# Kernel optimization log

Hardware: AMD Instinct MI355X
Metric: run time of the kernel (lower is better)

The kernel has to match this reference:

```python
import jax, jax.numpy as jnp
import numpy as np

B, T, D, H = 2, 2048, 1024, 16
DH = D // H


def setup_inputs() -> dict:
    key = jax.random.key(0)
    ks = jax.random.split(key, 8)
    s = 1.0 / np.sqrt(D)  # xavier-ish scale
    return {
        "query": jax.random.normal(ks[0], (B, T, D), jnp.float32),
        "key": jax.random.normal(ks[1], (B, T, D), jnp.float32),
        "value": jax.random.normal(ks[2], (B, T, D), jnp.float32),
        "Wq": jax.random.normal(ks[3], (D, D), jnp.float32) * s,
        "bq": jnp.zeros((D,), jnp.float32),
        "Wk": jax.random.normal(ks[4], (D, D), jnp.float32) * s,
        "bk": jnp.zeros((D,), jnp.float32),
        "Wv": jax.random.normal(ks[5], (D, D), jnp.float32) * s,
        "bv": jnp.zeros((D,), jnp.float32),
        "Wo": jax.random.normal(ks[6], (D, D), jnp.float32) * s,
        "bo": jnp.zeros((D,), jnp.float32),
        # causal mask (B, T, T); True = attend
        "mask": jnp.broadcast_to(jnp.tril(jnp.ones((T, T), bool)), (B, T, T)),
    }


def _split_heads(x):  # (B, T, D) -> (B, H, T, Dh)
    return x.reshape(B, T, H, DH).transpose(0, 2, 1, 3)


def reference(query, key, value, Wq, bq, Wk, bk, Wv, bv, Wo, bo, mask):
    q = _split_heads(query @ Wq + bq)
    k = _split_heads(key @ Wk + bk)
    v = _split_heads(value @ Wv + bv)
    scores = jnp.einsum("bhqd,bhkd->bhqk", q, k) / jnp.sqrt(jnp.float32(DH))
    scores = jnp.where(mask[:, None, :, :], scores, -jnp.inf)
    w = jax.nn.softmax(scores, axis=-1)
    out = jnp.einsum("bhqk,bhkd->bhqd", w, v)
    out = out.transpose(0, 2, 1, 3).reshape(B, T, D)  # merge heads
    return out @ Wo + bo
```

## Files before the change

kernel.cpp:

```cpp
#include <hip/hip_runtime.h>

typedef unsigned short u16;
typedef __attribute__((ext_vector_type(4))) float f32x4;
typedef __attribute__((ext_vector_type(8))) short bf16x8;

#define MFMA16(a,b,c) __builtin_amdgcn_mfma_f32_16x16x32_bf16((a),(b),(c),0,0,0)

__device__ inline u16 f2bf(float f){
  union { float f; unsigned u; } v; v.f = f;
  unsigned r = v.u + 0x7FFFu + ((v.u >> 16) & 1u);
  return (u16)(r >> 16);
}
__device__ inline void storeC(float* p, float v){ *p = v; }
__device__ inline void storeC(u16* p, float v){ *p = f2bf(v); }

typedef const __attribute__((address_space(1))) unsigned int* gas_ptr;
typedef __attribute__((address_space(3))) unsigned int* las_ptr;
__device__ inline void gload_lds16(const u16* g, u16* l){
  __builtin_amdgcn_global_load_lds((gas_ptr)(const void*)g, (las_ptr)(void*)l, 16, 0, 0);
}

template<int N>
__device__ inline float rorf(float v){
  union { float f; int i; } a, b; a.f = v;
  b.i = __builtin_amdgcn_update_dpp(a.i, a.i, 0x120|N, 0xF, 0xF, false);
  return b.f;
}
__device__ inline float redMax16(float v){
  v = fmaxf(v, rorf<8>(v)); v = fmaxf(v, rorf<4>(v));
  v = fmaxf(v, rorf<2>(v)); v = fmaxf(v, rorf<1>(v));
  return v;
}
__device__ inline float redSum16(float v){
  v += rorf<8>(v); v += rorf<4>(v); v += rorf<2>(v); v += rorf<1>(v);
  return v;
}

struct CvtArgs { const float* x[3]; u16* y[3]; };
__global__ void k_cvt3(CvtArgs a, int n4){
  const float* x = a.x[blockIdx.y];
  u16* y = a.y[blockIdx.y];
  int i = blockIdx.x*blockDim.x + threadIdx.x;
  if (i < n4){
    float4 v = ((const float4*)x)[i];
    ushort4 o;
    o.x = f2bf(v.x); o.y = f2bf(v.y); o.z = f2bf(v.z); o.w = f2bf(v.w);
    ((ushort4*)y)[i] = o;
  }
}

struct TwbArgs { const float* W[4]; u16* Wt[4]; };
__global__ void k_twb4(TwbArgs a){
  __shared__ u16 t[32][33];
  const float* W = a.W[blockIdx.z];
  u16* Wt = a.Wt[blockIdx.z];
  int kb = blockIdx.x*32, nb = blockIdx.y*32;
  int tx = threadIdx.x, ty = threadIdx.y;
  #pragma unroll
  for (int i=0;i<32;i+=8)
    t[ty+i][tx] = f2bf(W[(size_t)(kb+ty+i)*1024 + nb+tx]);
  __syncthreads();
  #pragma unroll
  for (int i=0;i<32;i+=8)
    Wt[(size_t)(nb+ty+i)*1024 + kb+tx] = t[tx][ty+i];
}

__global__ void k_tv(const u16* __restrict__ V, u16* __restrict__ VT){
  __shared__ u16 t[32][33];
  int tb = blockIdx.x*32;
  int db = blockIdx.y*32;
  int bh = blockIdx.z;
  int b = bh>>4, h = bh&15;
  int tx = threadIdx.x, ty = threadIdx.y;
  #pragma unroll
  for (int i=0;i<32;i+=8)
    t[ty+i][tx] = V[(size_t)(b*2048 + tb+ty+i)*1024 + h*64 + db+tx];
  __syncthreads();
  #pragma unroll
  for (int i=0;i<32;i+=8)
    VT[(size_t)(bh*64 + db+ty+i)*2048 + tb+tx] = t[tx][ty+i];
}

template<typename OutT>
__device__ inline void gemm_body(const u16* __restrict__ A, const u16* __restrict__ Bt,
                                 const float* __restrict__ bias, OutT* __restrict__ C,
                                 int bx, int by){
  const int N=1024, K=1024;
  __shared__ __attribute__((aligned(16))) u16 As[128*64];
  __shared__ __attribute__((aligned(16))) u16 Bs[128*64];
  const int tid  = threadIdx.x;
  const int wave = tid>>6, lane = tid&63;
  const int lo = lane&15, hi = lane>>4;
  const int row0 = bx*128, col0 = by*128;
  const int wm = (wave>>1)*64, wn = (wave&1)*64;
  f32x4 acc[4][4];
  #pragma unroll
  for (int i=0;i<4;i++)
    #pragma unroll
    for (int j=0;j<4;j++) acc[i][j] = (f32x4){0.f,0.f,0.f,0.f};

  for (int k0=0; k0<K; k0+=64){
    #pragma unroll
    for (int r=0;r<4;r++){
      int c = r*256 + tid;
      gload_lds16(A  + (size_t)(row0 + (c>>3))*K + k0 + (c&7)*8, As + c*8);
      gload_lds16(Bt + (size_t)(col0 + (c>>3))*K + k0 + (c&7)*8, Bs + c*8);
    }
    __syncthreads();
    __builtin_amdgcn_s_setprio(1);
    #pragma unroll
    for (int ks=0;ks<2;ks++){
      bf16x8 af[4], bfr[4];
      #pragma unroll
      for (int mf=0;mf<4;mf++)
        af[mf] = *(const bf16x8*)(As + (wm+mf*16+lo)*64 + ks*32 + hi*8);
      #pragma unroll
      for (int nf=0;nf<4;nf++)
        bfr[nf] = *(const bf16x8*)(Bs + (wn+nf*16+lo)*64 + ks*32 + hi*8);
      #pragma unroll
      for (int mf=0;mf<4;mf++)
        #pragma unroll
        for (int nf=0;nf<4;nf++)
          acc[mf][nf] = MFMA16(af[mf], bfr[nf], acc[mf][nf]);
    }
    __builtin_amdgcn_s_setprio(0);
    __syncthreads();
  }
  #pragma unroll
  for (int mf=0;mf<4;mf++){
    #pragma unroll
    for (int nf=0;nf<4;nf++){
      int r0 = row0 + wm + mf*16 + hi*4;
      int c0 = col0 + wn + nf*16 + lo;
      float bb = bias[c0];
      #pragma unroll
      for (int r=0;r<4;r++)
        storeC(&C[(size_t)(r0+r)*N + c0], acc[mf][nf][r] + bb);
    }
  }
}

struct GemmArgs3 { const u16* A[3]; const u16* Bt[3]; const float* bias[3]; u16* C[3]; };
__global__ __launch_bounds__(256) void k_gemm3(GemmArgs3 g){
  int flat = blockIdx.x + (blockIdx.y<<5) + (blockIdx.z<<8);
  int swz = (flat&7)*96 + (flat>>3);
  int by = swz & 7, bx = (swz>>3) & 31, bz = swz >> 8;
  gemm_body<u16>(g.A[bz], g.Bt[bz], g.bias[bz], g.C[bz], bx, by);
}
__global__ __launch_bounds__(256) void k_gemmO(const u16* __restrict__ A, const u16* __restrict__ Bt,
                                               const float* __restrict__ bias, float* __restrict__ C){
  int flat = blockIdx.x + (blockIdx.y<<5);
  int swz = (flat&7)*32 + (flat>>3);
  int by = swz & 7, bx = swz >> 3;
  gemm_body<float>(A, Bt, bias, C, bx, by);
}

__global__ __launch_bounds__(256) void k_attn(
    const u16* __restrict__ Q, const u16* __restrict__ Kp,
    const u16* __restrict__ VT, u16* __restrict__ O)
{
  const int T=2048, D=1024, NT=32;
  __shared__ __attribute__((aligned(16))) u16 Ks[2][64*64];
  __shared__ __attribute__((aligned(16))) u16 Vs[2][64*64];
  __shared__ __attribute__((aligned(16))) u16 Plds[4][16*64];
  int flat = blockIdx.x + (blockIdx.y<<4);
  int swz = (flat&7)*64 + (flat>>3);
  const int xb = swz & 15;
  const int bh = swz >> 4;
  const int b = bh>>4, h = bh&15;
  const int tid = threadIdx.x;
  const int wave = tid>>6, lane = tid&63;
  const int lo = lane&15, hi = lane>>4;
  const float NEG = -__builtin_inff();
  const float sc = 0.125f * 1.44269504f;

  const int cof0 = ((hi    ) ^ (lo&7))*8;
  const int cof1 = ((hi + 4) ^ (lo&7))*8;

  const int c0 = tid, c1 = 256 + tid;
  const int sr0 = c0>>3, sj0 = (c0&7)^(sr0&7);
  const int sr1 = c1>>3, sj1 = (c1&7)^(sr1&7);
  const u16* Kbase = Kp + (size_t)(b*T)*D + h*64;
  const u16* Vbase = VT + (size_t)(bh*64)*T;
  const size_t kOff0 = (size_t)sr0*D + sj0*8, kOff1 = (size_t)sr1*D + sj1*8;
  const size_t vOff0 = (size_t)sr0*T + sj0*8, vOff1 = (size_t)sr1*T + sj1*8;

  for (int half=0; half<2; half++){
    const int qb = half ? (NT-1-xb) : xb;
    const int qrow0 = qb*64 + wave*16;
    const u16* Qb = Q + (size_t)(b*T + qrow0 + lo)*D + h*64;
    bf16x8 qf0 = *(const bf16x8*)(Qb + hi*8);
    bf16x8 qf1 = *(const bf16x8*)(Qb + 32 + hi*8);

    f32x4 o[4];
    #pragma unroll
    for (int nf=0;nf<4;nf++) o[nf] = (f32x4){0.f,0.f,0.f,0.f};
    float m[4], l[4];
    #pragma unroll
    for (int r=0;r<4;r++){ m[r] = NEG; l[r] = 0.f; }

    gload_lds16(Kbase + kOff0, &Ks[0][c0*8]);
    gload_lds16(Kbase + kOff1, &Ks[0][c1*8]);
    gload_lds16(Vbase + vOff0, &Vs[0][c0*8]);
    gload_lds16(Vbase + vOff1, &Vs[0][c1*8]);
    __syncthreads();

    int cur = 0;
    for (int kb=0; kb<=qb; kb++){
      if (kb < qb){
        const u16* Kt = Kbase + (size_t)(kb+1)*64*D;
        const u16* Vt = Vbase + (kb+1)*64;
        gload_lds16(Kt + kOff0, &Ks[cur^1][c0*8]);
        gload_lds16(Kt + kOff1, &Ks[cur^1][c1*8]);
        gload_lds16(Vt + vOff0, &Vs[cur^1][c0*8]);
        gload_lds16(Vt + vOff1, &Vs[cur^1][c1*8]);
      }
      const u16* Kl = Ks[cur];
      const u16* Vl = Vs[cur];
      f32x4 s[4];
      __builtin_amdgcn_s_setprio(1);
      #pragma unroll
      for (int nf=0;nf<4;nf++){
        int row = nf*16 + lo;
        bf16x8 kf0 = *(const bf16x8*)(Kl + row*64 + cof0);
        bf16x8 kf1 = *(const bf16x8*)(Kl + row*64 + cof1);
        f32x4 z = (f32x4){0.f,0.f,0.f,0.f};
        z = MFMA16(qf0, kf0, z);
        s[nf] = MFMA16(qf1, kf1, z);
      }
      __builtin_amdgcn_s_setprio(0);
      float ls[4][4];
      float pm[4] = {NEG,NEG,NEG,NEG};
      if (kb == qb){
        #pragma unroll
        for (int nf=0;nf<4;nf++){
          int col = kb*64 + nf*16 + lo;
          #pragma unroll
          for (int r=0;r<4;r++){
            int row = qrow0 + hi*4 + r;
            float v = s[nf][r]*sc;
            if (col > row) v = NEG;
            ls[nf][r] = v;
            pm[r] = fmaxf(pm[r], v);
          }
        }
      } else {
        #pragma unroll
        for (int nf=0;nf<4;nf++)
          #pragma unroll
          for (int r=0;r<4;r++){
            float v = s[nf][r]*sc;
            ls[nf][r] = v;
            pm[r] = fmaxf(pm[r], v);
          }
      }
      #pragma unroll
      for (int r=0;r<4;r++) pm[r] = redMax16(pm[r]);
      bool small = true;
      #pragma unroll
      for (int r=0;r<4;r++) small = small && (pm[r] <= m[r] + 8.f);
      const bool resc = !__all(small);
      float alpha[4];
      if (resc){
        #pragma unroll
        for (int r=0;r<4;r++){
          float mn = fmaxf(m[r], pm[r]);
          alpha[r] = __builtin_amdgcn_exp2f(m[r] - mn);
          m[r] = mn;
        }
      }
      float rs[4] = {0.f,0.f,0.f,0.f};
      #pragma unroll
      for (int nf=0;nf<4;nf++)
        #pragma unroll
        for (int r=0;r<4;r++){
          float p = __builtin_amdgcn_exp2f(ls[nf][r] - m[r]);
          rs[r] += p;
          int prow = hi*4+r, pcol = nf*16+lo;
          Plds[wave][prow*64 + (pcol ^ ((prow&7)<<3))] = f2bf(p);
        }
      #pragma unroll
      for (int r=0;r<4;r++) rs[r] = redSum16(rs[r]);
      if (resc){
        #pragma unroll
        for (int r=0;r<4;r++) l[r] = l[r]*alpha[r] + rs[r];
        #pragma unroll
        for (int nf=0;nf<4;nf++)
          #pragma unroll
          for (int r=0;r<4;r++) o[nf][r] *= alpha[r];
      } else {
        #pragma unroll
        for (int r=0;r<4;r++) l[r] += rs[r];
      }
      bf16x8 pa0 = *(const bf16x8*)(&Plds[wave][lo*64 + cof0]);
      bf16x8 pa1 = *(const bf16x8*)(&Plds[wave][lo*64 + cof1]);
      __builtin_amdgcn_s_setprio(1);
      #pragma unroll
      for (int nf=0;nf<4;nf++){
        int row = nf*16 + lo;
        bf16x8 v0 = *(const bf16x8*)(Vl + row*64 + cof0);
        bf16x8 v1 = *(const bf16x8*)(Vl + row*64 + cof1);
        o[nf] = MFMA16(pa0, v0, o[nf]);
        o[nf] = MFMA16(pa1, v1, o[nf]);
      }
      __builtin_amdgcn_s_setprio(0);
      __syncthreads();
      cur ^= 1;
    }
    #pragma unroll
    for (int nf=0;nf<4;nf++)
      #pragma unroll
      for (int r=0;r<4;r++){
        int row = qrow0 + hi*4 + r;
        O[(size_t)(b*T+row)*D + h*64 + nf*16 + lo] = f2bf(o[nf][r] / l[r]);
      }
  }
}

extern "C" void kernel_launch(void* const* d_in, const int* in_sizes, int n_in,
                              void* d_out, int out_size, void* d_ws, size_t ws_size,
                              hipStream_t stream) {
  const int B=2, T=2048, D=1024;
  const int M = B*T;
  const float* query = (const float*)d_in[0];
  const float* key   = (const float*)d_in[1];
  const float* value = (const float*)d_in[2];
  const float* Wq = (const float*)d_in[3];  const float* bq = (const float*)d_in[4];
  const float* Wk = (const float*)d_in[5];  const float* bk = (const float*)d_in[6];
  const float* Wv = (const float*)d_in[7];  const float* bv = (const float*)d_in[8];
  const float* Wo = (const float*)d_in[9];  const float* bo = (const float*)d_in[10];
  float* out = (float*)d_out;

  char* ws = (char*)d_ws;
  const size_t MB = 1024*1024;
  u16* xq  = (u16*)(ws + 0*MB);
  u16* xk  = (u16*)(ws + 8*MB);
  u16* xv  = (u16*)(ws + 16*MB);
  u16* WqT = (u16*)(ws + 24*MB);
  u16* WkT = (u16*)(ws + 26*MB);
  u16* WvT = (u16*)(ws + 28*MB);
  u16* WoT = (u16*)(ws + 30*MB);
  u16* Qp  = (u16*)(ws + 32*MB);
  u16* Kp  = (u16*)(ws + 40*MB);
  u16* Vp  = (u16*)(ws + 48*MB);
  u16* VTp = (u16*)(ws + 56*MB);
  u16* AO  = (u16*)(ws + 64*MB);

  int n4 = M*D/4;
  CvtArgs ca; ca.x[0]=query; ca.x[1]=key; ca.x[2]=value; ca.y[0]=xq; ca.y[1]=xk; ca.y[2]=xv;
  k_cvt3<<<dim3(n4/256, 3), 256, 0, stream>>>(ca, n4);

  TwbArgs ta; ta.W[0]=Wq; ta.W[1]=Wk; ta.W[2]=Wv; ta.W[3]=Wo;
  ta.Wt[0]=WqT; ta.Wt[1]=WkT; ta.Wt[2]=WvT; ta.Wt[3]=WoT;
  k_twb4<<<dim3(32,32,4), dim3(32,8), 0, stream>>>(ta);

  GemmArgs3 ga;
  ga.A[0]=xq; ga.A[1]=xk; ga.A[2]=xv;
  ga.Bt[0]=WqT; ga.Bt[1]=WkT; ga.Bt[2]=WvT;
  ga.bias[0]=bq; ga.bias[1]=bk; ga.bias[2]=bv;
  ga.C[0]=Qp; ga.C[1]=Kp; ga.C[2]=Vp;
  k_gemm3<<<dim3(32,8,3), 256, 0, stream>>>(ga);

  k_tv<<<dim3(T/32, 2, 32), dim3(32,8), 0, stream>>>(Vp, VTp);
  k_attn<<<dim3(16, 32), 256, 0, stream>>>(Qp, Kp, VTp, AO);
  k_gemmO<<<dim3(32,8), 256, 0, stream>>>(AO, WoT, bo, out);
}
```

Baseline: 141.6 us.

## Split attention into one block per query tile and offload row sums to MFMA

The attention kernel no longer pairs two query tiles per block for causal load balancing. It launches one block per (batch-head, query tile), ordered longest-first with an XCD-aware mapping. The softmax row-sum is computed with an MFMA against a ones vector instead of DPP reductions. Scaling is folded into an fma inside exp2, with a lazy-rescale threshold in unscaled units, and a cheaper round-to-nearest bf16 conversion replaces ties-to-even. This doubles the block count to fill more CUs and cuts VALU work per tile, at the cost of relying on hardware block scheduling for imbalance and slightly different rounding.

New measurement: 132.3 us. -6.6%, faster.

```diff
diff --git a/kernel.cpp b/kernel.cpp
--- a/kernel.cpp
+++ b/kernel.cpp
@@ -10,6 +10,10 @@
   union { float f; unsigned u; } v; v.f = f;
   unsigned r = v.u + 0x7FFFu + ((v.u >> 16) & 1u);
   return (u16)(r >> 16);
+}
+__device__ inline u16 f2bf_fast(float f){
+  union { float f; unsigned u; } v; v.f = f;
+  return (u16)((v.u + 0x8000u) >> 16);
 }
 __device__ inline void storeC(float* p, float v){ *p = v; }
 __device__ inline void storeC(u16* p, float v){ *p = f2bf(v); }
@@ -29,10 +33,6 @@
 __device__ inline float redMax16(float v){
   v = fmaxf(v, rorf<8>(v)); v = fmaxf(v, rorf<4>(v));
   v = fmaxf(v, rorf<2>(v)); v = fmaxf(v, rorf<1>(v));
-  return v;
-}
-__device__ inline float redSum16(float v){
-  v += rorf<8>(v); v += rorf<4>(v); v += rorf<2>(v); v += rorf<1>(v);
   return v;
 }
 
@@ -159,20 +159,21 @@
     const u16* __restrict__ Q, const u16* __restrict__ Kp,
     const u16* __restrict__ VT, u16* __restrict__ O)
 {
-  const int T=2048, D=1024, NT=32;
+  const int T=2048, D=1024;
   __shared__ __attribute__((aligned(16))) u16 Ks[2][64*64];
   __shared__ __attribute__((aligned(16))) u16 Vs[2][64*64];
   __shared__ __attribute__((aligned(16))) u16 Plds[4][16*64];
-  int flat = blockIdx.x + (blockIdx.y<<4);
-  int swz = (flat&7)*64 + (flat>>3);
-  const int xb = swz & 15;
-  const int bh = swz >> 4;
+  int f = blockIdx.x + (blockIdx.y<<5);
+  int xcd = f & 7, idx = f >> 3;
+  const int bh = (xcd<<2) | (idx&3);
+  const int qb = 31 - (idx>>2);
   const int b = bh>>4, h = bh&15;
   const int tid = threadIdx.x;
   const int wave = tid>>6, lane = tid&63;
   const int lo = lane&15, hi = lane>>4;
   const float NEG = -__builtin_inff();
   const float sc = 0.125f * 1.44269504f;
+  const bf16x8 ones = {0x3F80,0x3F80,0x3F80,0x3F80,0x3F80,0x3F80,0x3F80,0x3F80};
 
   const int cof0 = ((hi    ) ^ (lo&7))*8;
   const int cof1 = ((hi + 4) ^ (lo&7))*8;
@@ -185,136 +186,129 @@
   const size_t kOff0 = (size_t)sr0*D + sj0*8, kOff1 = (size_t)sr1*D + sj1*8;
   const size_t vOff0 = (size_t)sr0*T + sj0*8, vOff1 = (size_t)sr1*T + sj1*8;
 
-  for (int half=0; half<2; half++){
-    const int qb = half ? (NT-1-xb) : xb;
-    const int qrow0 = qb*64 + wave*16;
-    const u16* Qb = Q + (size_t)(b*T + qrow0 + lo)*D + h*64;
-    bf16x8 qf0 = *(const bf16x8*)(Qb + hi*8);
-    bf16x8 qf1 = *(const bf16x8*)(Qb + 32 + hi*8);
-
-    f32x4 o[4];
-    #pragma unroll
-    for (int nf=0;nf<4;nf++) o[nf] = (f32x4){0.f,0.f,0.f,0.f};
-    float m[4], l[4];
-    #pragma unroll
-    for (int r=0;r<4;r++){ m[r] = NEG; l[r] = 0.f; }
-
-    gload_lds16(Kbase + kOff0, &Ks[0][c0*8]);
-    gload_lds16(Kbase + kOff1, &Ks[0][c1*8]);
-    gload_lds16(Vbase + vOff0, &Vs[0][c0*8]);
-    gload_lds16(Vbase + vOff1, &Vs[0][c1*8]);
-    __syncthreads();
-
-    int cur = 0;
-    for (int kb=0; kb<=qb; kb++){
-      if (kb < qb){
-        const u16* Kt = Kbase + (size_t)(kb+1)*64*D;
-        const u16* Vt = Vbase + (kb+1)*64;
-        gload_lds16(Kt + kOff0, &Ks[cur^1][c0*8]);
-        gload_lds16(Kt + kOff1, &Ks[cur^1][c1*8]);
-        gload_lds16(Vt + vOff0, &Vs[cur^1][c0*8]);
-        gload_lds16(Vt + vOff1, &Vs[cur^1][c1*8]);
-      }
-      const u16* Kl = Ks[cur];
-      const u16* Vl = Vs[cur];
-      f32x4 s[4];
-      __builtin_amdgcn_s_setprio(1);
+  const int qrow0 = qb*64 + wave*16;
+  const u16* Qb = Q + (size_t)(b*T + qrow0 + lo)*D + h*64;
+  bf16x8 qf0 = *(const bf16x8*)(Qb + hi*8);
+  bf16x8 qf1 = *(const bf16x8*)(Qb + 32 + hi*8);
+
+  f32x4 o[4];
+  #pragma unroll
+  for (int nf=0;nf<4;nf++) o[nf] = (f32x4){0.f,0.f,0.f,0.f};
+  float m[4], l[4];
+  #pragma unroll
+  for (int r=0;r<4;r++){ m[r] = NEG; l[r] = 0.f; }
+
+  gload_lds16(Kbase + kOff0, &Ks[0][c0*8]);
+  gload_lds16(Kbase + kOff1, &Ks[0][c1*8]);
+  gload_lds16(Vbase + vOff0, &Vs[0][c0*8]);
+  gload_lds16(Vbase + vOff1, &Vs[0][c1*8]);
+  __syncthreads();
+
+  int cur = 0;
+  for (int kb=0; kb<=qb; kb++){
+    if (kb < qb){
+      const u16* Kt = Kbase + (size_t)(kb+1)*64*D;
+      const u16* Vt = Vbase + (kb+1)*64;
+      gload_lds16(Kt + kOff0, &Ks[cur^1][c0*8]);
+      gload_lds16(Kt + kOff1, &Ks[cur^1][c1*8]);
+      gload_lds16(Vt + vOff0, &Vs[cur^1][c0*8]);
+      gload_lds16(Vt + vOff1, &Vs[cur^1][c1*8]);
+    }
+    const u16* Kl = Ks[cur];
+    const u16* Vl = Vs[cur];
+    f32x4 s[4];
+    __builtin_amdgcn_s_setprio(1);
+    #pragma unroll
+    for (int nf=0;nf<4;nf++){
+      int row = nf*16 + lo;
+      bf16x8 kf0 = *(const bf16x8*)(Kl + row*64 + cof0);
+      bf16x8 kf1 = *(const bf16x8*)(Kl + row*64 + cof1);
+      f32x4 z = (f32x4){0.f,0.f,0.f,0.f};
+      z = MFMA16(qf0, kf0, z);
+      s[nf] = MFMA16(qf1, kf1, z);
+    }
+    __builtin_amdgcn_s_setprio(0);
+    float pm[4] = {NEG,NEG,NEG,NEG};
+    if (kb == qb){
       #pragma unroll
       for (int nf=0;nf<4;nf++){
-        int row = nf*16 + lo;
-        bf16x8 kf0 = *(const bf16x8*)(Kl + row*64 + cof0);
-        bf16x8 kf1 = *(const bf16x8*)(Kl + row*64 + cof1);
-        f32x4 z = (f32x4){0.f,0.f,0.f,0.f};
-        z = MFMA16(qf0, kf0, z);
-        s[nf] = MFMA16(qf1, kf1, z);
-      }
-      __builtin_amdgcn_s_setprio(0);
-      float ls[4][4];
-      float pm[4] = {NEG,NEG,NEG,NEG};
-      if (kb == qb){
-        #pragma unroll
-        for (int nf=0;nf<4;nf++){
-          int col = kb*64 + nf*16 + lo;
-          #pragma unroll
-          for (int r=0;r<4;r++){
-            int row = qrow0 + hi*4 + r;
-            float v = s[nf][r]*sc;
-            if (col > row) v = NEG;
-            ls[nf][r] = v;
-            pm[r] = fmaxf(pm[r], v);
-          }
-        }
-      } else {
-        #pragma unroll
-        for (int nf=0;nf<4;nf++)
-          #pragma unroll
-          for (int r=0;r<4;r++){
-            float v = s[nf][r]*sc;
-            ls[nf][r] = v;
-            pm[r] = fmaxf(pm[r], v);
-          }
-      }
-      #pragma unroll
-      for (int r=0;r<4;r++) pm[r] = redMax16(pm[r]);
-      bool small = true;
-      #pragma unroll
-      for (int r=0;r<4;r++) small = small && (pm[r] <= m[r] + 8.f);
-      const bool resc = !__all(small);
-      float alpha[4];
-      if (resc){
+        int col = kb*64 + nf*16 + lo;
         #pragma unroll
         for (int r=0;r<4;r++){
-          float mn = fmaxf(m[r], pm[r]);
-          alpha[r] = __builtin_amdgcn_exp2f(m[r] - mn);
-          m[r] = mn;
+          int row = qrow0 + hi*4 + r;
+          if (col > row) s[nf][r] = NEG;
+          pm[r] = fmaxf(pm[r], s[nf][r]);
         }
       }
-      float rs[4] = {0.f,0.f,0.f,0.f};
+    } else {
       #pragma unroll
       for (int nf=0;nf<4;nf++)
         #pragma unroll
-        for (int r=0;r<4;r++){
-          float p = __builtin_amdgcn_exp2f(ls[nf][r] - m[r]);
-          rs[r] += p;
-          int prow = hi*4+r, pcol = nf*16+lo;
-          Plds[wave][prow*64 + (pcol ^ ((prow&7)<<3))] = f2bf(p);
-        }
-      #pragma unroll
-      for (int r=0;r<4;r++) rs[r] = redSum16(rs[r]);
-      if (resc){
+        for (int r=0;r<4;r++)
+          pm[r] = fmaxf(pm[r], s[nf][r]);
+    }
+    #pragma unroll
+    for (int r=0;r<4;r++) pm[r] = redMax16(pm[r]);
+    bool small = true;
+    #pragma unroll
+    for (int r=0;r<4;r++) small = small && (pm[r] <= m[r] + 44.f);
+    const bool resc = !__all(small);
+    float alpha[4];
+    if (resc){
+      #pragma unroll
+      for (int r=0;r<4;r++){
+        float mn = fmaxf(m[r], pm[r]);
+        alpha[r] = __builtin_amdgcn_exp2f((m[r] - mn)*sc);
+        m[r] = mn;
+      }
+      #pragma unroll
+      for (int nf=0;nf<4;nf++)
         #pragma unroll
-        for (int r=0;r<4;r++) l[r] = l[r]*alpha[r] + rs[r];
-        #pragma unroll
-        for (int nf=0;nf<4;nf++)
-          #pragma unroll
-          for (int r=0;r<4;r++) o[nf][r] *= alpha[r];
-      } else {
-        #pragma unroll
-        for (int r=0;r<4;r++) l[r] += rs[r];
+        for (int r=0;r<4;r++) o[nf][r] *= alpha[r];
+    }
+    float msc[4];
+    #pragma unroll
+    for (int r=0;r<4;r++) msc[r] = m[r]*sc;
+    #pragma unroll
+    for (int nf=0;nf<4;nf++)
+      #pragma unroll
+      for (int r=0;r<4;r++){
+        float p = __builtin_amdgcn_exp2f(__builtin_fmaf(s[nf][r], sc, -msc[r]));
+        int prow = hi*4+r, pcol = nf*16+lo;
+        Plds[wave][prow*64 + (pcol ^ ((prow&7)<<3))] = f2bf_fast(p);
       }
-      bf16x8 pa0 = *(const bf16x8*)(&Plds[wave][lo*64 + cof0]);
-      bf16x8 pa1 = *(const bf16x8*)(&Plds[wave][lo*64 + cof1]);
-      __builtin_amdgcn_s_setprio(1);
-      #pragma unroll
-      for (int nf=0;nf<4;nf++){
-        int row = nf*16 + lo;
-        bf16x8 v0 = *(const bf16x8*)(Vl + row*64 + cof0);
-        bf16x8 v1 = *(const bf16x8*)(Vl + row*64 + cof1);
-        o[nf] = MFMA16(pa0, v0, o[nf]);
-        o[nf] = MFMA16(pa1, v1, o[nf]);
-      }
-      __builtin_amdgcn_s_setprio(0);
-      __syncthreads();
-      cur ^= 1;
-    }
-    #pragma unroll
-    for (int nf=0;nf<4;nf++)
-      #pragma unroll
-      for (int r=0;r<4;r++){
-        int row = qrow0 + hi*4 + r;
-        O[(size_t)(b*T+row)*D + h*64 + nf*16 + lo] = f2bf(o[nf][r] / l[r]);
-      }
+    bf16x8 pa0 = *(const bf16x8*)(&Plds[wave][lo*64 + cof0]);
+    bf16x8 pa1 = *(const bf16x8*)(&Plds[wave][lo*64 + cof1]);
+    f32x4 lsum = (f32x4){0.f,0.f,0.f,0.f};
+    __builtin_amdgcn_s_setprio(1);
+    lsum = MFMA16(pa0, ones, lsum);
+    lsum = MFMA16(pa1, ones, lsum);
+    #pragma unroll
+    for (int nf=0;nf<4;nf++){
+      int row = nf*16 + lo;
+      bf16x8 v0 = *(const bf16x8*)(Vl + row*64 + cof0);
+      bf16x8 v1 = *(const bf16x8*)(Vl + row*64 + cof1);
+      o[nf] = MFMA16(pa0, v0, o[nf]);
+      o[nf] = MFMA16(pa1, v1, o[nf]);
+    }
+    __builtin_amdgcn_s_setprio(0);
+    if (resc){
+      #pragma unroll
+      for (int r=0;r<4;r++) l[r] = l[r]*alpha[r] + lsum[r];
+    } else {
+      #pragma unroll
+      for (int r=0;r<4;r++) l[r] += lsum[r];
+    }
+    __syncthreads();
+    cur ^= 1;
   }
+  #pragma unroll
+  for (int nf=0;nf<4;nf++)
+    #pragma unroll
+    for (int r=0;r<4;r++){
+      int row = qrow0 + hi*4 + r;
+      O[(size_t)(b*T+row)*D + h*64 + nf*16 + lo] = f2bf_fast(o[nf][r] / l[r]);
+    }
 }
 
 extern "C" void kernel_launch(void* const* d_in, const int* in_sizes, int n_in,
@@ -362,6 +356,6 @@
   k_gemm3<<<dim3(32,8,3), 256, 0, stream>>>(ga);
 
   k_tv<<<dim3(T/32, 2, 32), dim3(32,8), 0, stream>>>(Vp, VTp);
-  k_attn<<<dim3(16, 32), 256, 0, stream>>>(Qp, Kp, VTp, AO);
+  k_attn<<<dim3(32,32), 256, 0, stream>>>(Qp, Kp, VTp, AO);
   k_gemmO<<<dim3(32,8), 256, 0, stream>>>(AO, WoT, bo, out);
 }
```
